# Optimization experiments

Measured on AMD Instinct MI355X. Metric: run time of the kernel, lower is better.

## Reference

```python
import jax, jax.numpy as jnp
import numpy as np


def _dwconv3(x, w, b):
    # Depthwise conv1d, kernel=3, 'same' padding, channels_first.
    # x: [B, Cs, L], w: [3, Cs], b: [Cs]
    xp = jnp.pad(x, ((0, 0), (0, 0), (1, 1)))
    return (w[0][:, None] * xp[:, :, :-2]
            + w[1][:, None] * xp[:, :, 1:-1]
            + w[2][:, None] * xp[:, :, 2:]
            + b[:, None])


def setup_inputs() -> dict:
    key = jax.random.key(0)
    ks = jax.random.split(key, 3)
    B, C, L, S = 32, 256, 4096, 8
    return {
        "inputs": jax.random.normal(ks[0], (B, C, L), jnp.float32),
        "conv_w": jax.random.normal(ks[1], (S, 3, C // S), jnp.float32) * 0.3,
        "conv_b": jnp.zeros((S, C // S), jnp.float32),
        "ln_gamma": jnp.ones((L,), jnp.float32),
        "ln_beta": jnp.zeros((L,), jnp.float32),
        "pw_w": jax.random.normal(ks[2], (C,), jnp.float32) * 0.3,
        "pw_b": jnp.zeros((C,), jnp.float32),
    }


def reference(inputs, conv_w, conv_b, ln_gamma, ln_beta, pw_w, pw_b):
    S = conv_w.shape[0]
    xs = jnp.split(inputs, S, axis=1)  # each [B, C/S, L]
    # sequential recurrence: y_i = dwconv_i(x_i + y_{i-1})
    y = _dwconv3(xs[0], conv_w[0], conv_b[0])
    ys = [y]
    for i in range(1, S):
        y = _dwconv3(xs[i] + y, conv_w[i], conv_b[i])
        ys.append(y)
    y = jnp.concatenate(ys, axis=1)  # [B, C, L]
    # keras LayerNormalization(axis=-1): normalize over time axis L
    mean = jnp.mean(y, axis=-1, keepdims=True)
    var = jnp.var(y, axis=-1, keepdims=True)
    y = (y - mean) * jax.lax.rsqrt(var + 1e-6) * ln_gamma + ln_beta
    # depthwise k=1 conv (per-channel scale + bias) then exact gelu
    y = jax.nn.gelu(y * pw_w[None, :, None] + pw_b[None, :, None], approximate=False)
    return inputs + y
```

## Files before the change

### kernel.cpp

```cpp
#include <hip/hip_runtime.h>
#include <math.h>

#define BB   32
#define CC   256
#define LL   4096
#define SS   8
#define CS   32
#define NT   256
#define F4_ROW (LL / 4)
#define F4_THR (F4_ROW / NT)

typedef float f4 __attribute__((ext_vector_type(4)));

__device__ __forceinline__ float gelu_exact(float x) {
    return 0.5f * x * (1.0f + erff(x * 0.70710678118654752440f));
}

__device__ __forceinline__ void lds_barrier() {
    asm volatile("s_waitcnt lgkmcnt(0)" ::: "memory");
    __builtin_amdgcn_s_barrier();
    asm volatile("" ::: "memory");
}

__global__ __launch_bounds__(NT, 4)
void hdconv_encoder_kernel(const float* __restrict__ inp,
                           const float* __restrict__ conv_w,
                           const float* __restrict__ conv_b,
                           const float* __restrict__ ln_g,
                           const float* __restrict__ ln_b,
                           const float* __restrict__ pw_w,
                           const float* __restrict__ pw_b,
                           float* __restrict__ out) {
    __shared__ float eW[2][17];
    __shared__ float eX[2][17];
    __shared__ float red[2][8];

    const int t    = threadIdx.x;
    const int blk  = blockIdx.x;
    const int b    = blk >> 5;
    const int c    = blk & 31;
    const int lane = t & 63;
    const int wave = t >> 6;

    if (t == 0) {
        eW[0][0]  = 0.0f; eW[1][0]  = 0.0f;
        eX[0][16] = 0.0f; eX[1][16] = 0.0f;
    }

    float y[16];
#pragma unroll
    for (int j = 0; j < 16; ++j) y[j] = 0.0f;

    float4 g4[F4_THR], e4[F4_THR];
    {
        const float4* gp = (const float4*)ln_g;
        const float4* ep = (const float4*)ln_b;
#pragma unroll
        for (int k = 0; k < F4_THR; ++k) {
            g4[k] = gp[t + NT * k];
            e4[k] = ep[t + NT * k];
        }
    }

    f4 x4[F4_THR];
    {
        const f4* xrow = (const f4*)(inp + ((size_t)(b * CC + c)) * LL);
#pragma unroll
        for (int k = 0; k < F4_THR; ++k) x4[k] = xrow[t + NT * k];
    }

#pragma unroll
    for (int k = 0; k < F4_THR; ++k) {
        const int kw = k * 4 + wave;
        if (lane == 63) eW[0][1 + kw] = x4[k].w;
        if (lane == 0)  eX[0][kw]     = x4[k].x;
    }
    lds_barrier();

    for (int i = 0; i < SS; ++i) {
        const int p  = i & 1;
        const int ch = i * CS + c;

        f4 xn4[F4_THR];
        if (i + 1 < SS) {
            const f4* xn = (const f4*)(inp + ((size_t)(b * CC + ch + CS)) * LL);
#pragma unroll
            for (int k = 0; k < F4_THR; ++k) xn4[k] = xn[t + NT * k];
        }

        const float w0 = conv_w[i * 96 + 0 * CS + c];
        const float w1 = conv_w[i * 96 + 1 * CS + c];
        const float w2 = conv_w[i * 96 + 2 * CS + c];
        const float bb = conv_b[i * CS + c];

        float lsum = 0.0f, lsq = 0.0f;
#pragma unroll
        for (int k = 0; k < F4_THR; ++k) {
            const int kw = k * 4 + wave;
            const float s0 = x4[k].x + y[4 * k + 0];
            const float s1 = x4[k].y + y[4 * k + 1];
            const float s2 = x4[k].z + y[4 * k + 2];
            const float s3 = x4[k].w + y[4 * k + 3];
            float sm1 = __shfl_up(s3, 1, 64);
            float sp4 = __shfl_down(s0, 1, 64);
            if (lane == 0)  sm1 = eW[p][kw];
            if (lane == 63) sp4 = eX[p][kw + 1];
            const float y0 = fmaf(w0, sm1, fmaf(w1, s0, fmaf(w2, s1, bb)));
            const float y1 = fmaf(w0, s0,  fmaf(w1, s1, fmaf(w2, s2, bb)));
            const float y2 = fmaf(w0, s1,  fmaf(w1, s2, fmaf(w2, s3, bb)));
            const float y3 = fmaf(w0, s2,  fmaf(w1, s3, fmaf(w2, sp4, bb)));
            y[4 * k + 0] = y0; y[4 * k + 1] = y1;
            y[4 * k + 2] = y2; y[4 * k + 3] = y3;
            lsum += (y0 + y1) + (y2 + y3);
            lsq  += fmaf(y0, y0, fmaf(y1, y1, fmaf(y2, y2, y3 * y3)));
        }

#pragma unroll
        for (int off = 32; off > 0; off >>= 1) {
            lsum += __shfl_down(lsum, off, 64);
            lsq  += __shfl_down(lsq,  off, 64);
        }
        if (lane == 0) { red[p][wave * 2] = lsum; red[p][wave * 2 + 1] = lsq; }

        if (i + 1 < SS) {
#pragma unroll
            for (int k = 0; k < F4_THR; ++k) {
                const int kw = k * 4 + wave;
                if (lane == 63) eW[p ^ 1][1 + kw] = xn4[k].w + y[4 * k + 3];
                if (lane == 0)  eX[p ^ 1][kw]     = xn4[k].x + y[4 * k + 0];
            }
        }

        lds_barrier();

        const float sum = (red[p][0] + red[p][2]) + (red[p][4] + red[p][6]);
        const float sq  = (red[p][1] + red[p][3]) + (red[p][5] + red[p][7]);
        const float mean = sum * (1.0f / LL);
        const float var  = sq * (1.0f / LL) - mean * mean;
        const float inv  = rsqrtf(var + 1e-6f);

        const float pw = pw_w[ch];
        const float pb = pw_b[ch];
        f4* orow = (f4*)(out + ((size_t)(b * CC + ch)) * LL);
#pragma unroll
        for (int k = 0; k < F4_THR; ++k) {
            f4 o;
            float n;
            n   = fmaf((y[4 * k + 0] - mean) * inv, g4[k].x, e4[k].x);
            o.x = x4[k].x + gelu_exact(fmaf(n, pw, pb));
            n   = fmaf((y[4 * k + 1] - mean) * inv, g4[k].y, e4[k].y);
            o.y = x4[k].y + gelu_exact(fmaf(n, pw, pb));
            n   = fmaf((y[4 * k + 2] - mean) * inv, g4[k].z, e4[k].z);
            o.z = x4[k].z + gelu_exact(fmaf(n, pw, pb));
            n   = fmaf((y[4 * k + 3] - mean) * inv, g4[k].w, e4[k].w);
            o.w = x4[k].w + gelu_exact(fmaf(n, pw, pb));
            __builtin_nontemporal_store(o, &orow[t + NT * k]);
        }

        if (i + 1 < SS) {
#pragma unroll
            for (int k = 0; k < F4_THR; ++k) x4[k] = xn4[k];
        }
    }
}

extern "C" void kernel_launch(void* const* d_in, const int* in_sizes, int n_in,
                              void* d_out, int out_size, void* d_ws, size_t ws_size,
                              hipStream_t stream) {
    const float* inp    = (const float*)d_in[0];
    const float* conv_w = (const float*)d_in[1];
    const float* conv_b = (const float*)d_in[2];
    const float* ln_g   = (const float*)d_in[3];
    const float* ln_b   = (const float*)d_in[4];
    const float* pw_w   = (const float*)d_in[5];
    const float* pw_b   = (const float*)d_in[6];
    float* out = (float*)d_out;

    dim3 grid(BB * CS);
    dim3 block(NT);
    hdconv_encoder_kernel<<<grid, block, 0, stream>>>(
        inp, conv_w, conv_b, ln_g, ln_b, pw_w, pw_b, out);
}
```

Baseline: 265.3 us.

## Double block size, stage LN params in LDS, exchange only y halos

Raises the block to 512 threads with launch bounds of 8, halving per-thread register arrays. LayerNorm gamma and beta move from registers into shared memory. Halo exchange now shares only the previous y boundary values through LDS, with x halos loaded directly from global memory. Nontemporal output stores become plain stores. This aims at higher occupancy to hide memory latency, at the cost of extra LDS traffic and scattered scalar halo loads.

```diff
diff --git a/kernel.cpp b/kernel.cpp
--- a/kernel.cpp
+++ b/kernel.cpp
@@ -6,11 +6,11 @@
 #define LL   4096
 #define SS   8
 #define CS   32
-#define NT   256
+#define NT   512
+#define WV   (NT / 64)
 #define F4_ROW (LL / 4)
 #define F4_THR (F4_ROW / NT)
-
-typedef float f4 __attribute__((ext_vector_type(4)));
+#define NCH    (F4_ROW / 64)
 
 __device__ __forceinline__ float gelu_exact(float x) {
     return 0.5f * x * (1.0f + erff(x * 0.70710678118654752440f));
@@ -22,7 +22,23 @@
     asm volatile("" ::: "memory");
 }
 
-__global__ __launch_bounds__(NT, 4)
+__device__ __forceinline__ void load_row(const float* __restrict__ rowf,
+                                         int t, int lane,
+                                         float4* x4, float* xhl, float* xhr) {
+    const float4* row4 = (const float4*)rowf;
+#pragma unroll
+    for (int k = 0; k < F4_THR; ++k) {
+        const int f = t + NT * k;
+        x4[k] = row4[f];
+        float hl = 0.0f, hr = 0.0f;
+        if (lane == 0  && f > 0)          hl = rowf[4 * f - 1];
+        if (lane == 63 && f < F4_ROW - 1) hr = rowf[4 * f + 4];
+        xhl[k] = hl;
+        xhr[k] = hr;
+    }
+}
+
+__global__ __launch_bounds__(NT, 8)
 void hdconv_encoder_kernel(const float* __restrict__ inp,
                            const float* __restrict__ conv_w,
                            const float* __restrict__ conv_b,
@@ -31,9 +47,11 @@
                            const float* __restrict__ pw_w,
                            const float* __restrict__ pw_b,
                            float* __restrict__ out) {
-    __shared__ float eW[2][17];
-    __shared__ float eX[2][17];
-    __shared__ float red[2][8];
+    __shared__ float4 Gs[F4_ROW];
+    __shared__ float4 Es[F4_ROW];
+    __shared__ float eYl[2][NCH + 1];
+    __shared__ float eYr[2][NCH + 1];
+    __shared__ float red[2][2 * WV];
 
     const int t    = threadIdx.x;
     const int blk  = blockIdx.x;
@@ -42,77 +60,67 @@
     const int lane = t & 63;
     const int wave = t >> 6;
 
-    if (t == 0) {
-        eW[0][0]  = 0.0f; eW[1][0]  = 0.0f;
-        eX[0][16] = 0.0f; eX[1][16] = 0.0f;
-    }
-
-    float y[16];
-#pragma unroll
-    for (int j = 0; j < 16; ++j) y[j] = 0.0f;
-
-    float4 g4[F4_THR], e4[F4_THR];
     {
         const float4* gp = (const float4*)ln_g;
         const float4* ep = (const float4*)ln_b;
 #pragma unroll
         for (int k = 0; k < F4_THR; ++k) {
-            g4[k] = gp[t + NT * k];
-            e4[k] = ep[t + NT * k];
+            Gs[t + NT * k] = gp[t + NT * k];
+            Es[t + NT * k] = ep[t + NT * k];
         }
     }
-
-    f4 x4[F4_THR];
-    {
-        const f4* xrow = (const f4*)(inp + ((size_t)(b * CC + c)) * LL);
-#pragma unroll
-        for (int k = 0; k < F4_THR; ++k) x4[k] = xrow[t + NT * k];
+    if (t < NCH + 1) {
+        eYl[0][t] = 0.0f; eYl[1][t] = 0.0f;
+        eYr[0][t] = 0.0f; eYr[1][t] = 0.0f;
     }
 
+    float y[4 * F4_THR];
 #pragma unroll
-    for (int k = 0; k < F4_THR; ++k) {
-        const int kw = k * 4 + wave;
-        if (lane == 63) eW[0][1 + kw] = x4[k].w;
-        if (lane == 0)  eX[0][kw]     = x4[k].x;
-    }
+    for (int j = 0; j < 4 * F4_THR; ++j) y[j] = 0.0f;
+
+    float4 x4[F4_THR];
+    float  xhl[F4_THR], xhr[F4_THR];
+    load_row(inp + ((size_t)(b * CC + c)) * LL, t, lane, x4, xhl, xhr);
+
     lds_barrier();
 
     for (int i = 0; i < SS; ++i) {
         const int p  = i & 1;
         const int ch = i * CS + c;
 
-        f4 xn4[F4_THR];
-        if (i + 1 < SS) {
-            const f4* xn = (const f4*)(inp + ((size_t)(b * CC + ch + CS)) * LL);
-#pragma unroll
-            for (int k = 0; k < F4_THR; ++k) xn4[k] = xn[t + NT * k];
-        }
+        float4 xn4[F4_THR];
+        float  xnl[F4_THR], xnr[F4_THR];
+        if (i + 1 < SS)
+            load_row(inp + ((size_t)(b * CC + ch + CS)) * LL, t, lane,
+                     xn4, xnl, xnr);
 
-        const float w0 = conv_w[i * 96 + 0 * CS + c];
-        const float w1 = conv_w[i * 96 + 1 * CS + c];
-        const float w2 = conv_w[i * 96 + 2 * CS + c];
-        const float bb = conv_b[i * CS + c];
+        const float w0  = conv_w[i * 96 + 0 * CS + c];
+        const float w1  = conv_w[i * 96 + 1 * CS + c];
+        const float w2  = conv_w[i * 96 + 2 * CS + c];
+        const float bcv = conv_b[i * CS + c];
 
         float lsum = 0.0f, lsq = 0.0f;
 #pragma unroll
         for (int k = 0; k < F4_THR; ++k) {
-            const int kw = k * 4 + wave;
+            const int kw = k * WV + wave;
             const float s0 = x4[k].x + y[4 * k + 0];
             const float s1 = x4[k].y + y[4 * k + 1];
             const float s2 = x4[k].z + y[4 * k + 2];
             const float s3 = x4[k].w + y[4 * k + 3];
             float sm1 = __shfl_up(s3, 1, 64);
             float sp4 = __shfl_down(s0, 1, 64);
-            if (lane == 0)  sm1 = eW[p][kw];
-            if (lane == 63) sp4 = eX[p][kw + 1];
-            const float y0 = fmaf(w0, sm1, fmaf(w1, s0, fmaf(w2, s1, bb)));
-            const float y1 = fmaf(w0, s0,  fmaf(w1, s1, fmaf(w2, s2, bb)));
-            const float y2 = fmaf(w0, s1,  fmaf(w1, s2, fmaf(w2, s3, bb)));
-            const float y3 = fmaf(w0, s2,  fmaf(w1, s3, fmaf(w2, sp4, bb)));
+            if (lane == 0)  sm1 = xhl[k] + eYl[p][kw];
+            if (lane == 63) sp4 = xhr[k] + eYr[p][kw + 1];
+            const float y0 = fmaf(w0, sm1, fmaf(w1, s0, fmaf(w2, s1, bcv)));
+            const float y1 = fmaf(w0, s0,  fmaf(w1, s1, fmaf(w2, s2, bcv)));
+            const float y2 = fmaf(w0, s1,  fmaf(w1, s2, fmaf(w2, s3, bcv)));
+            const float y3 = fmaf(w0, s2,  fmaf(w1, s3, fmaf(w2, sp4, bcv)));
             y[4 * k + 0] = y0; y[4 * k + 1] = y1;
             y[4 * k + 2] = y2; y[4 * k + 3] = y3;
             lsum += (y0 + y1) + (y2 + y3);
             lsq  += fmaf(y0, y0, fmaf(y1, y1, fmaf(y2, y2, y3 * y3)));
+            if (lane == 63) eYl[p ^ 1][1 + kw] = y3;
+            if (lane == 0)  eYr[p ^ 1][kw]     = y0;
         }
 
 #pragma unroll
@@ -122,44 +130,41 @@
         }
         if (lane == 0) { red[p][wave * 2] = lsum; red[p][wave * 2 + 1] = lsq; }
 
-        if (i + 1 < SS) {
-#pragma unroll
-            for (int k = 0; k < F4_THR; ++k) {
-                const int kw = k * 4 + wave;
-                if (lane == 63) eW[p ^ 1][1 + kw] = xn4[k].w + y[4 * k + 3];
-                if (lane == 0)  eX[p ^ 1][kw]     = xn4[k].x + y[4 * k + 0];
-            }
-        }
-
         lds_barrier();
 
-        const float sum = (red[p][0] + red[p][2]) + (red[p][4] + red[p][6]);
-        const float sq  = (red[p][1] + red[p][3]) + (red[p][5] + red[p][7]);
+        const float sum = ((red[p][0]  + red[p][2])  + (red[p][4]  + red[p][6]))
+                        + ((red[p][8]  + red[p][10]) + (red[p][12] + red[p][14]));
+        const float sq  = ((red[p][1]  + red[p][3])  + (red[p][5]  + red[p][7]))
+                        + ((red[p][9]  + red[p][11]) + (red[p][13] + red[p][15]));
         const float mean = sum * (1.0f / LL);
         const float var  = sq * (1.0f / LL) - mean * mean;
         const float inv  = rsqrtf(var + 1e-6f);
 
         const float pw = pw_w[ch];
         const float pb = pw_b[ch];
-        f4* orow = (f4*)(out + ((size_t)(b * CC + ch)) * LL);
+        float4* orow = (float4*)(out + ((size_t)(b * CC + ch)) * LL);
 #pragma unroll
         for (int k = 0; k < F4_THR; ++k) {
-            f4 o;
+            const float4 g = Gs[t + NT * k];
+            const float4 e = Es[t + NT * k];
+            float4 o;
             float n;
-            n   = fmaf((y[4 * k + 0] - mean) * inv, g4[k].x, e4[k].x);
+            n   = fmaf((y[4 * k + 0] - mean) * inv, g.x, e.x);
             o.x = x4[k].x + gelu_exact(fmaf(n, pw, pb));
-            n   = fmaf((y[4 * k + 1] - mean) * inv, g4[k].y, e4[k].y);
+            n   = fmaf((y[4 * k + 1] - mean) * inv, g.y, e.y);
             o.y = x4[k].y + gelu_exact(fmaf(n, pw, pb));
-            n   = fmaf((y[4 * k + 2] - mean) * inv, g4[k].z, e4[k].z);
+            n   = fmaf((y[4 * k + 2] - mean) * inv, g.z, e.z);
             o.z = x4[k].z + gelu_exact(fmaf(n, pw, pb));
-            n   = fmaf((y[4 * k + 3] - mean) * inv, g4[k].w, e4[k].w);
+            n   = fmaf((y[4 * k + 3] - mean) * inv, g.w, e.w);
             o.w = x4[k].w + gelu_exact(fmaf(n, pw, pb));
-            __builtin_nontemporal_store(o, &orow[t + NT * k]);
+            orow[t + NT * k] = o;
         }
 
         if (i + 1 < SS) {
 #pragma unroll
-            for (int k = 0; k < F4_THR; ++k) x4[k] = xn4[k];
+            for (int k = 0; k < F4_THR; ++k) {
+                x4[k] = xn4[k]; xhl[k] = xnl[k]; xhr[k] = xnr[k];
+            }
         }
     }
 }
```

Result: slower. 302.7 us (+14.1%).
